# Kernel optimization log

Measured on AMD Instinct MI355X. Metric: run time of the kernel, lower is better.

Reference implementation:

```python
import jax, jax.numpy as jnp
import numpy as np

GROUP = 64  # group_size for precision='int4'


def setup_inputs() -> dict:
    key = jax.random.key(0)
    ks = jax.random.split(key, 7)
    B, S, C, O, R = 64, 4, 8192, 8192, 32
    x = jax.random.normal(ks[0], (B, S, C), dtype=jnp.float32)
    # unpacked int4 weight values stored as int32 codes in [0,16) -> value = code - 8
    qweight = jax.random.randint(ks[1], (O, C), 0, 16, dtype=jnp.int32)
    wscales = jax.random.uniform(ks[2], (C // GROUP, O), dtype=jnp.float32,
                                 minval=0.005, maxval=0.02)
    # smoothing factors kept strictly positive and away from zero
    smooth_factor = jax.random.uniform(ks[3], (C,), dtype=jnp.float32,
                                       minval=0.5, maxval=1.5)
    proj_down = jax.random.normal(ks[4], (C, R), dtype=jnp.float32) * 0.02
    proj_up = jax.random.normal(ks[5], (O, R), dtype=jnp.float32) * 0.02
    bias = jax.random.normal(ks[6], (O,), dtype=jnp.float32) * 0.01
    return {"x": x, "qweight": qweight, "wscales": wscales,
            "smooth_factor": smooth_factor, "proj_down": proj_down,
            "proj_up": proj_up, "bias": bias}


def reference(x, qweight, wscales, smooth_factor, proj_down, proj_up, bias):
    B, S, C = x.shape
    O = qweight.shape[0]
    ng = C // GROUP
    xr = x.reshape(B * S, C)

    # SVD low-rank correction: lora_act = x @ proj_down ; out += lora_act @ proj_up^T
    lora = (xr @ proj_down) @ proj_up.T  # (M, O)

    # activation smoothing + per-group symmetric int4 quantization
    xs = xr / smooth_factor                                   # (M, C)
    xg = xs.reshape(-1, ng, GROUP)                            # (M, ng, 64)
    ascales = jnp.max(jnp.abs(xg), axis=-1, keepdims=True) / 7.0
    ascales = jnp.maximum(ascales, 1e-8)
    q_act = jnp.clip(jnp.round(xg / ascales), -8.0, 7.0)
    x_deq = (q_act * ascales).reshape(-1, C)                  # dequantized act

    # per-group weight dequant: wscales is (ng, O)
    w = (qweight.astype(jnp.float32) - 8.0).reshape(O, ng, GROUP)
    w_deq = (w * wscales.T[:, :, None]).reshape(O, C)         # (O, C)

    out = x_deq @ w_deq.T + lora + bias                       # (M, O)
    return out.reshape(B, S, O)
```

## Files before the change

### kernel.cpp

```cpp
#include <hip/hip_runtime.h>
#include <stdint.h>

#define C_DIM 8192
#define O_DIM 8192
#define M_DIM 256
#define NG    128
#define RK    32
#define SUPS  16
#define GPS   8

typedef float f32x4 __attribute__((ext_vector_type(4)));
typedef int   i32x4 __attribute__((ext_vector_type(4)));
typedef unsigned int u32;

__device__ __forceinline__ void gll16(const void* g, void* l) {
  __builtin_amdgcn_global_load_lds(
      (const __attribute__((address_space(1))) void*)g,
      (__attribute__((address_space(3))) void*)l, 16, 0, 0);
}
__device__ __forceinline__ int pack8(i32x4 r) {
  return (r[0] & 0xff) | ((r[1] & 0xff) << 8) | ((r[2] & 0xff) << 16) |
         (r[3] << 24);
}

__global__ __launch_bounds__(256) void k_lora(const float* __restrict__ x,
                                              const float* __restrict__ pd,
                                              float* __restrict__ lact) {
  const int t  = threadIdx.x;
  const int rq = t & 7;
  const int kc = (t >> 3) & 15;
  const int ml = t >> 7;
  const int m  = blockIdx.x * 2 + ml;
  const float* xrow = x + (size_t)m * C_DIM + kc * 512;
  const float* pdp  = pd + (size_t)(kc * 512) * RK + rq * 4;
  float a0 = 0.f, a1 = 0.f, a2 = 0.f, a3 = 0.f;
  for (int k = 0; k < 512; k += 4) {
    float4 xv = *(const float4*)(xrow + k);
    float4 p0 = *(const float4*)(pdp + (size_t)(k + 0) * RK);
    float4 p1 = *(const float4*)(pdp + (size_t)(k + 1) * RK);
    float4 p2 = *(const float4*)(pdp + (size_t)(k + 2) * RK);
    float4 p3 = *(const float4*)(pdp + (size_t)(k + 3) * RK);
    a0 += xv.x * p0.x + xv.y * p1.x + xv.z * p2.x + xv.w * p3.x;
    a1 += xv.x * p0.y + xv.y * p1.y + xv.z * p2.y + xv.w * p3.y;
    a2 += xv.x * p0.z + xv.y * p1.z + xv.z * p2.z + xv.w * p3.z;
    a3 += xv.x * p0.w + xv.y * p1.w + xv.z * p2.w + xv.w * p3.w;
  }
  __shared__ float red[2][8][16][4];
  red[ml][rq][kc][0] = a0;
  red[ml][rq][kc][1] = a1;
  red[ml][rq][kc][2] = a2;
  red[ml][rq][kc][3] = a3;
  __syncthreads();
  if (t < 64) {
    const int ml2 = t >> 5, r = t & 31, rq2 = r >> 2, j = r & 3;
    float s = 0.f;
#pragma unroll
    for (int c = 0; c < 16; ++c) s += red[ml2][rq2][c][j];
    lact[(size_t)(blockIdx.x * 2 + ml2) * RK + r] = s;
  }
}

__global__ __launch_bounds__(256) void k_prep(const float* __restrict__ x,
                                              const float* __restrict__ smooth,
                                              float* __restrict__ scp,
                                              i32x4* __restrict__ wsA8) {
  const int t    = threadIdx.x;
  const int ml   = t & 15;
  const int gl   = t >> 4;
  const int MT   = blockIdx.x >> 3;
  const int gblk = blockIdx.x & 7;
  const int m = MT * 16 + ml;
  const int g = gblk * 16 + gl;
  const float* xp = x + (size_t)m * C_DIM + g * 64;
  const float* sp = smooth + g * 64;
  float xs[64];
  float amax = 0.0f;
#pragma unroll
  for (int i = 0; i < 64; i += 4) {
    float4 xv = *(const float4*)(xp + i);
    float4 sv = *(const float4*)(sp + i);
    xs[i + 0] = xv.x / sv.x;
    xs[i + 1] = xv.y / sv.y;
    xs[i + 2] = xv.z / sv.z;
    xs[i + 3] = xv.w / sv.w;
    amax = fmaxf(amax, fabsf(xs[i + 0]));
    amax = fmaxf(amax, fabsf(xs[i + 1]));
    amax = fmaxf(amax, fabsf(xs[i + 2]));
    amax = fmaxf(amax, fabsf(xs[i + 3]));
  }
  const float ascale = fmaxf(amax / 7.0f, 1e-8f);
  int qi[64];
  int rs = 0;
#pragma unroll
  for (int i = 0; i < 64; ++i) {
    float qv = fminf(fmaxf(rintf(xs[i] / ascale), -8.0f), 7.0f);
    qi[i] = (int)qv;
    rs += qi[i];
  }
  scp[(size_t)g * 512 + m]       = ascale;
  scp[(size_t)g * 512 + 256 + m] = 8.0f * (float)rs * ascale;
  const size_t base = ((size_t)(MT * NG + g)) * 64;
#pragma unroll
  for (int lg = 0; lg < 4; ++lg) {
    const int* q = qi + lg * 16;
    i32x4 c;
#pragma unroll
    for (int dw = 0; dw < 4; ++dw)
      c[dw] = (q[dw * 4 + 0] & 0xff) | ((q[dw * 4 + 1] & 0xff) << 8) |
              ((q[dw * 4 + 2] & 0xff) << 16) | (q[dw * 4 + 3] << 24);
    wsA8[base + lg * 16 + ml] = c;
  }
}

__global__ __launch_bounds__(512, 4) void k_main(
    const int* __restrict__ qw, const float* __restrict__ wsc,
    const float* __restrict__ pu, const float* __restrict__ bias,
    const float* __restrict__ scp, const i32x4* __restrict__ wsA8,
    const float* __restrict__ lact, float* __restrict__ out) {
  const int t    = threadIdx.x;
  const int n0   = blockIdx.x * 16;
  const int w    = t >> 6;
  const int l    = t & 63;
  const int lrow = l >> 4;
  const int lcol = l & 15;

  __shared__ char  ldsB[2][16][512];
  __shared__ float ldsSC[2][4096];
  __shared__ float ldsW[NG * 16];

  for (int i = t; i < NG * 16; i += 512)
    ldsW[i] = wsc[(size_t)(i >> 4) * O_DIM + n0 + (i & 15)];

  const int sr = t >> 5, cg = t & 31;
  const int* gB = qw + (size_t)(n0 + sr) * C_DIM + cg * 16;
  const int wslot = (cg ^ (sr & 7)) * 16;
  const char* gSCb = (const char*)scp;
  const i32x4* gA0 = wsA8 + ((size_t)(w * 2 + 0) * NG) * 64 + l;
  const i32x4* gA1 = wsA8 + ((size_t)(w * 2 + 1) * NG) * 64 + l;

  f32x4 acc0 = (f32x4){0.f, 0.f, 0.f, 0.f};
  f32x4 acc1 = (f32x4){0.f, 0.f, 0.f, 0.f};
  const i32x4 z = (i32x4){0, 0, 0, 0};

  i32x4 br0, br1, br2, br3;
  i32x4 R0_0, R0_1, R1_0, R1_1, R2_0, R2_1, R3_0, R3_1;

  __syncthreads();

  br0 = __builtin_nontemporal_load((const i32x4*)(gB + 0));
  br1 = __builtin_nontemporal_load((const i32x4*)(gB + 4));
  br2 = __builtin_nontemporal_load((const i32x4*)(gB + 8));
  br3 = __builtin_nontemporal_load((const i32x4*)(gB + 12));
  gll16(gSCb + t * 16, &ldsSC[0][t * 4]);
  gll16(gSCb + 8192 + t * 16, &ldsSC[0][2048 + t * 4]);
  R0_0 = gA0[0 * 64];  R0_1 = gA1[0 * 64];
  R1_0 = gA0[1 * 64];  R1_1 = gA1[1 * 64];
  R2_0 = gA0[2 * 64];  R2_1 = gA1[2 * 64];
  R3_0 = gA0[3 * 64];  R3_1 = gA1[3 * 64];
  asm volatile("s_waitcnt vmcnt(8)" ::: "memory");
  {
    i32x4 pk = (i32x4){pack8(br0), pack8(br1), pack8(br2), pack8(br3)};
    *(i32x4*)&ldsB[0][sr][wslot] = pk;
  }
  asm volatile("s_waitcnt lgkmcnt(0)" ::: "memory");
  __builtin_amdgcn_s_barrier();

#define SUBJ(J, RA, RB, VMC)                                                   \
  {                                                                            \
    asm volatile("s_waitcnt vmcnt(" #VMC ")" ::: "memory");                    \
    i32x4 bf = *(const i32x4*)&ldsB[s & 1][lcol]                               \
                   [(((J) * 4 + lrow) ^ (lcol & 7)) * 16];                     \
    f32x4 as0 = *(const f32x4*)&ldsSC[s & 1][(J) * 512 + (w * 2 + 0) * 16 +    \
                                             lrow * 4];                        \
    f32x4 rs0 = *(const f32x4*)&ldsSC[s & 1][(J) * 512 + 256 +                 \
                                             (w * 2 + 0) * 16 + lrow * 4];     \
    f32x4 as1 = *(const f32x4*)&ldsSC[s & 1][(J) * 512 + (w * 2 + 1) * 16 +    \
                                             lrow * 4];                        \
    f32x4 rs1 = *(const f32x4*)&ldsSC[s & 1][(J) * 512 + 256 +                 \
                                             (w * 2 + 1) * 16 + lrow * 4];     \
    const float wsv = ldsW[(s * GPS + (J)) * 16 + lcol];                       \
    i32x4 d0 = __builtin_amdgcn_mfma_i32_16x16x64_i8(RA, bf, z, 0, 0, 0);      \
    i32x4 d1 = __builtin_amdgcn_mfma_i32_16x16x64_i8(RB, bf, z, 0, 0, 0);      \
    int gn = s * GPS + (J) + 4;                                                \
    if (gn > NG - 1) gn = NG - 1;                                              \
    RA = gA0[(size_t)gn * 64];                                                 \
    RB = gA1[(size_t)gn * 64];                                                 \
    f32x4 df0, df1;                                                            \
    df0[0] = (float)d0[0]; df0[1] = (float)d0[1];                              \
    df0[2] = (float)d0[2]; df0[3] = (float)d0[3];                              \
    df1[0] = (float)d1[0]; df1[1] = (float)d1[1];                              \
    df1[2] = (float)d1[2]; df1[3] = (float)d1[3];                              \
    acc0 += wsv * (as0 * df0 - rs0);                                           \
    acc1 += wsv * (as1 * df1 - rs1);                                           \
  }

  for (int s = 0; s < SUPS; ++s) {
    const int sn = (s < SUPS - 1) ? s + 1 : SUPS - 1;
    const int nb = (s + 1) & 1;
    br0 = __builtin_nontemporal_load((const i32x4*)(gB + sn * 512 + 0));
    br1 = __builtin_nontemporal_load((const i32x4*)(gB + sn * 512 + 4));
    br2 = __builtin_nontemporal_load((const i32x4*)(gB + sn * 512 + 8));
    br3 = __builtin_nontemporal_load((const i32x4*)(gB + sn * 512 + 12));
    gll16(gSCb + (size_t)sn * 16384 + t * 16, &ldsSC[nb][t * 4]);
    gll16(gSCb + (size_t)sn * 16384 + 8192 + t * 16, &ldsSC[nb][2048 + t * 4]);

    SUBJ(0, R0_0, R0_1, 12)
    SUBJ(1, R1_0, R1_1, 12)
    SUBJ(2, R2_0, R2_1, 12)
    SUBJ(3, R3_0, R3_1, 12)
    SUBJ(4, R0_0, R0_1, 6)
    SUBJ(5, R1_0, R1_1, 6)
    SUBJ(6, R2_0, R2_1, 6)
    SUBJ(7, R3_0, R3_1, 6)

    asm volatile("s_waitcnt vmcnt(8)" ::: "memory");
    i32x4 pk = (i32x4){pack8(br0), pack8(br1), pack8(br2), pack8(br3)};
    *(i32x4*)&ldsB[nb][sr][wslot] = pk;
    asm volatile("s_waitcnt lgkmcnt(0)" ::: "memory");
    __builtin_amdgcn_s_barrier();
  }
#undef SUBJ

  const int n = n0 + lcol;
  const float bv = bias[n];
  float4 puq[8];
#pragma unroll
  for (int rq = 0; rq < 8; ++rq)
    puq[rq] = *(const float4*)(pu + (size_t)n * RK + rq * 4);
#pragma unroll
  for (int mi = 0; mi < 2; ++mi) {
    const f32x4 av = (mi == 0) ? acc0 : acc1;
#pragma unroll
    for (int j = 0; j < 4; ++j) {
      const int m = (w * 2 + mi) * 16 + lrow * 4 + j;
      const float* lp = lact + (size_t)m * RK;
      float lo = 0.f;
#pragma unroll
      for (int rq = 0; rq < 8; ++rq) {
        float4 lv = *(const float4*)(lp + rq * 4);
        lo += lv.x * puq[rq].x + lv.y * puq[rq].y + lv.z * puq[rq].z +
              lv.w * puq[rq].w;
      }
      out[(size_t)m * O_DIM + n] = av[j] + bv + lo;
    }
  }
}

extern "C" void kernel_launch(void* const* d_in, const int* in_sizes, int n_in,
                              void* d_out, int out_size, void* d_ws,
                              size_t ws_size, hipStream_t stream) {
  const float* x      = (const float*)d_in[0];
  const int*   qw     = (const int*)d_in[1];
  const float* wsc    = (const float*)d_in[2];
  const float* smooth = (const float*)d_in[3];
  const float* pd     = (const float*)d_in[4];
  const float* pu     = (const float*)d_in[5];
  const float* bias   = (const float*)d_in[6];
  float* out = (float*)d_out;

  char* ws = (char*)d_ws;
  float* lact = (float*)ws;
  float* scp  = (float*)(ws + 32 * 1024);
  i32x4* wsA8 = (i32x4*)(ws + 288 * 1024);

  hipLaunchKernelGGL(k_prep, dim3(128), dim3(256), 0, stream, x, smooth, scp,
                     wsA8);
  hipLaunchKernelGGL(k_lora, dim3(128), dim3(256), 0, stream, x, pd, lact);
  hipLaunchKernelGGL(k_main, dim3(512), dim3(512), 0, stream, qw, wsc, pu,
                     bias, scp, wsA8, lact, out);
}
```

Measured before the change: 163.5 us.

## Split K across two blocks with wider N tiles and add reduction kernel

Each k_main block now covers 32 output columns and half of the K range, so every activation fragment feeds four MFMAs instead of two and A reuse doubles. Partial sums go to two workspace planes, and a new k_red kernel adds them together with the LoRA correction and bias. The weight LDS tile changes from an XOR swizzle to a padded 528-byte row stride, and weight loads are no longer nontemporal. The cost is an extra kernel launch and roughly 16 MB of extra partial-sum traffic.

```diff
diff --git a/kernel.cpp b/kernel.cpp
--- a/kernel.cpp
+++ b/kernel.cpp
@@ -5,9 +5,9 @@
 #define O_DIM 8192
 #define M_DIM 256
 #define NG    128
+#define NGH   64
+#define SUPS  8
 #define RK    32
-#define SUPS  16
-#define GPS   8
 
 typedef float f32x4 __attribute__((ext_vector_type(4)));
 typedef int   i32x4 __attribute__((ext_vector_type(4)));
@@ -18,9 +18,8 @@
       (const __attribute__((address_space(1))) void*)g,
       (__attribute__((address_space(3))) void*)l, 16, 0, 0);
 }
-__device__ __forceinline__ int pack8(i32x4 r) {
-  return (r[0] & 0xff) | ((r[1] & 0xff) << 8) | ((r[2] & 0xff) << 16) |
-         (r[3] << 24);
+__device__ __forceinline__ int pack4(int a, int b, int c, int d) {
+  return (a & 0xff) | ((b & 0xff) << 8) | ((c & 0xff) << 16) | (d << 24);
 }
 
 __global__ __launch_bounds__(256) void k_lora(const float* __restrict__ x,
@@ -106,143 +105,192 @@
     i32x4 c;
 #pragma unroll
     for (int dw = 0; dw < 4; ++dw)
-      c[dw] = (q[dw * 4 + 0] & 0xff) | ((q[dw * 4 + 1] & 0xff) << 8) |
-              ((q[dw * 4 + 2] & 0xff) << 16) | (q[dw * 4 + 3] << 24);
+      c[dw] = pack4(q[dw * 4 + 0], q[dw * 4 + 1], q[dw * 4 + 2], q[dw * 4 + 3]);
     wsA8[base + lg * 16 + ml] = c;
   }
 }
 
 __global__ __launch_bounds__(512, 4) void k_main(
     const int* __restrict__ qw, const float* __restrict__ wsc,
-    const float* __restrict__ pu, const float* __restrict__ bias,
     const float* __restrict__ scp, const i32x4* __restrict__ wsA8,
-    const float* __restrict__ lact, float* __restrict__ out) {
+    float* __restrict__ P) {
   const int t    = threadIdx.x;
-  const int n0   = blockIdx.x * 16;
+  const int bid  = blockIdx.x;
+  const int kh   = bid & 1;
+  const int n0   = (bid >> 1) * 32;
+  const int g0   = kh * NGH;
   const int w    = t >> 6;
   const int l    = t & 63;
   const int lrow = l >> 4;
   const int lcol = l & 15;
 
-  __shared__ char  ldsB[2][16][512];
+  __shared__ char  ldsB[2][32 * 528];
   __shared__ float ldsSC[2][4096];
-  __shared__ float ldsW[NG * 16];
-
-  for (int i = t; i < NG * 16; i += 512)
-    ldsW[i] = wsc[(size_t)(i >> 4) * O_DIM + n0 + (i & 15)];
-
-  const int sr = t >> 5, cg = t & 31;
-  const int* gB = qw + (size_t)(n0 + sr) * C_DIM + cg * 16;
-  const int wslot = (cg ^ (sr & 7)) * 16;
-  const char* gSCb = (const char*)scp;
-  const i32x4* gA0 = wsA8 + ((size_t)(w * 2 + 0) * NG) * 64 + l;
-  const i32x4* gA1 = wsA8 + ((size_t)(w * 2 + 1) * NG) * 64 + l;
-
-  f32x4 acc0 = (f32x4){0.f, 0.f, 0.f, 0.f};
-  f32x4 acc1 = (f32x4){0.f, 0.f, 0.f, 0.f};
-  const i32x4 z = (i32x4){0, 0, 0, 0};
-
-  i32x4 br0, br1, br2, br3;
+  __shared__ float ldsW[NGH * 32];
+
+  for (int i = t; i < NGH * 32; i += 512)
+    ldsW[i] = wsc[(size_t)(g0 + (i >> 5)) * O_DIM + n0 + (i & 31)];
+
+  const int sr = t >> 4, sc = t & 15;
+  const int* gB = qw + (size_t)(n0 + sr) * C_DIM + kh * 4096 + sc * 32;
+  const float* gSC = scp + (size_t)g0 * 512 + t * 4;
+  const int wOff = sr * 528 + sc * 32;
+  const i32x4* gA0 = wsA8 + ((size_t)(w * 2 + 0) * NG + g0) * 64 + l;
+  const i32x4* gA1 = wsA8 + ((size_t)(w * 2 + 1) * NG + g0) * 64 + l;
+
+  __syncthreads();
+
+  i32x4 br0, br1, br2, br3, br4, br5, br6, br7;
   i32x4 R0_0, R0_1, R1_0, R1_1, R2_0, R2_1, R3_0, R3_1;
 
-  __syncthreads();
-
-  br0 = __builtin_nontemporal_load((const i32x4*)(gB + 0));
-  br1 = __builtin_nontemporal_load((const i32x4*)(gB + 4));
-  br2 = __builtin_nontemporal_load((const i32x4*)(gB + 8));
-  br3 = __builtin_nontemporal_load((const i32x4*)(gB + 12));
-  gll16(gSCb + t * 16, &ldsSC[0][t * 4]);
-  gll16(gSCb + 8192 + t * 16, &ldsSC[0][2048 + t * 4]);
+#define LOADB(S)                                                               \
+  br0 = *(const i32x4*)(gB + (S) * 512 + 0);                                   \
+  br1 = *(const i32x4*)(gB + (S) * 512 + 4);                                   \
+  br2 = *(const i32x4*)(gB + (S) * 512 + 8);                                   \
+  br3 = *(const i32x4*)(gB + (S) * 512 + 12);                                  \
+  br4 = *(const i32x4*)(gB + (S) * 512 + 16);                                  \
+  br5 = *(const i32x4*)(gB + (S) * 512 + 20);                                  \
+  br6 = *(const i32x4*)(gB + (S) * 512 + 24);                                  \
+  br7 = *(const i32x4*)(gB + (S) * 512 + 28);
+#define LOADSC(S, BUF)                                                         \
+  gll16(gSC + (size_t)(S) * 4096, &ldsSC[BUF][t * 4]);                         \
+  gll16(gSC + (size_t)(S) * 4096 + 2048, &ldsSC[BUF][2048 + t * 4]);
+#define PACKW(BUF)                                                             \
+  {                                                                            \
+    i32x4 pk0, pk1;                                                            \
+    pk0[0] = pack4(br0[0], br0[1], br0[2], br0[3]);                            \
+    pk0[1] = pack4(br1[0], br1[1], br1[2], br1[3]);                            \
+    pk0[2] = pack4(br2[0], br2[1], br2[2], br2[3]);                            \
+    pk0[3] = pack4(br3[0], br3[1], br3[2], br3[3]);                            \
+    pk1[0] = pack4(br4[0], br4[1], br4[2], br4[3]);                            \
+    pk1[1] = pack4(br5[0], br5[1], br5[2], br5[3]);                            \
+    pk1[2] = pack4(br6[0], br6[1], br6[2], br6[3]);                            \
+    pk1[3] = pack4(br7[0], br7[1], br7[2], br7[3]);                            \
+    *(i32x4*)&ldsB[BUF][wOff] = pk0;                                           \
+    *(i32x4*)&ldsB[BUF][wOff + 16] = pk1;                                      \
+  }
+
+  LOADB(0)
+  LOADSC(0, 0)
   R0_0 = gA0[0 * 64];  R0_1 = gA1[0 * 64];
   R1_0 = gA0[1 * 64];  R1_1 = gA1[1 * 64];
   R2_0 = gA0[2 * 64];  R2_1 = gA1[2 * 64];
   R3_0 = gA0[3 * 64];  R3_1 = gA1[3 * 64];
   asm volatile("s_waitcnt vmcnt(8)" ::: "memory");
-  {
-    i32x4 pk = (i32x4){pack8(br0), pack8(br1), pack8(br2), pack8(br3)};
-    *(i32x4*)&ldsB[0][sr][wslot] = pk;
-  }
+  PACKW(0)
   asm volatile("s_waitcnt lgkmcnt(0)" ::: "memory");
   __builtin_amdgcn_s_barrier();
 
-#define SUBJ(J, RA, RB, VMC)                                                   \
+  f32x4 acc00 = (f32x4){0.f, 0.f, 0.f, 0.f};
+  f32x4 acc01 = (f32x4){0.f, 0.f, 0.f, 0.f};
+  f32x4 acc10 = (f32x4){0.f, 0.f, 0.f, 0.f};
+  f32x4 acc11 = (f32x4){0.f, 0.f, 0.f, 0.f};
+  const i32x4 z = (i32x4){0, 0, 0, 0};
+
+#define SUBJ(J, RA0, RA1, VMC)                                                 \
   {                                                                            \
     asm volatile("s_waitcnt vmcnt(" #VMC ")" ::: "memory");                    \
-    i32x4 bf = *(const i32x4*)&ldsB[s & 1][lcol]                               \
-                   [(((J) * 4 + lrow) ^ (lcol & 7)) * 16];                     \
-    f32x4 as0 = *(const f32x4*)&ldsSC[s & 1][(J) * 512 + (w * 2 + 0) * 16 +    \
-                                             lrow * 4];                        \
-    f32x4 rs0 = *(const f32x4*)&ldsSC[s & 1][(J) * 512 + 256 +                 \
-                                             (w * 2 + 0) * 16 + lrow * 4];     \
-    f32x4 as1 = *(const f32x4*)&ldsSC[s & 1][(J) * 512 + (w * 2 + 1) * 16 +    \
-                                             lrow * 4];                        \
-    f32x4 rs1 = *(const f32x4*)&ldsSC[s & 1][(J) * 512 + 256 +                 \
-                                             (w * 2 + 1) * 16 + lrow * 4];     \
-    const float wsv = ldsW[(s * GPS + (J)) * 16 + lcol];                       \
-    i32x4 d0 = __builtin_amdgcn_mfma_i32_16x16x64_i8(RA, bf, z, 0, 0, 0);      \
-    i32x4 d1 = __builtin_amdgcn_mfma_i32_16x16x64_i8(RB, bf, z, 0, 0, 0);      \
-    int gn = s * GPS + (J) + 4;                                                \
-    if (gn > NG - 1) gn = NG - 1;                                              \
-    RA = gA0[(size_t)gn * 64];                                                 \
-    RB = gA1[(size_t)gn * 64];                                                 \
-    f32x4 df0, df1;                                                            \
-    df0[0] = (float)d0[0]; df0[1] = (float)d0[1];                              \
-    df0[2] = (float)d0[2]; df0[3] = (float)d0[3];                              \
-    df1[0] = (float)d1[0]; df1[1] = (float)d1[1];                              \
-    df1[2] = (float)d1[2]; df1[3] = (float)d1[3];                              \
-    acc0 += wsv * (as0 * df0 - rs0);                                           \
-    acc1 += wsv * (as1 * df1 - rs1);                                           \
+    const char* bb = &ldsB[s & 1][0];                                          \
+    i32x4 bf0 = *(const i32x4*)(bb + lcol * 528 + (J) * 64 + lrow * 16);       \
+    i32x4 bf1 = *(const i32x4*)(bb + (16 + lcol) * 528 + (J) * 64 + lrow * 16);\
+    const float* scb = &ldsSC[s & 1][(J) * 512];                               \
+    f32x4 as0 = *(const f32x4*)(scb + (w * 2 + 0) * 16 + lrow * 4);            \
+    f32x4 rs0 = *(const f32x4*)(scb + 256 + (w * 2 + 0) * 16 + lrow * 4);      \
+    f32x4 as1 = *(const f32x4*)(scb + (w * 2 + 1) * 16 + lrow * 4);            \
+    f32x4 rs1 = *(const f32x4*)(scb + 256 + (w * 2 + 1) * 16 + lrow * 4);      \
+    const float wsv0 = ldsW[(s * 8 + (J)) * 32 + lcol];                        \
+    const float wsv1 = ldsW[(s * 8 + (J)) * 32 + 16 + lcol];                   \
+    i32x4 d00 = __builtin_amdgcn_mfma_i32_16x16x64_i8(RA0, bf0, z, 0, 0, 0);   \
+    i32x4 d01 = __builtin_amdgcn_mfma_i32_16x16x64_i8(RA0, bf1, z, 0, 0, 0);   \
+    i32x4 d10 = __builtin_amdgcn_mfma_i32_16x16x64_i8(RA1, bf0, z, 0, 0, 0);   \
+    i32x4 d11 = __builtin_amdgcn_mfma_i32_16x16x64_i8(RA1, bf1, z, 0, 0, 0);   \
+    {                                                                          \
+      int lgn = s * 8 + (J) + 4;                                               \
+      if (lgn > NGH - 1) lgn = NGH - 1;                                        \
+      RA0 = gA0[(size_t)lgn * 64];                                             \
+      RA1 = gA1[(size_t)lgn * 64];                                             \
+    }                                                                          \
+    f32x4 df;                                                                  \
+    df[0] = (float)d00[0]; df[1] = (float)d00[1];                              \
+    df[2] = (float)d00[2]; df[3] = (float)d00[3];                              \
+    acc00 += wsv0 * (as0 * df - rs0);                                          \
+    df[0] = (float)d01[0]; df[1] = (float)d01[1];                              \
+    df[2] = (float)d01[2]; df[3] = (float)d01[3];                              \
+    acc01 += wsv1 * (as0 * df - rs0);                                          \
+    df[0] = (float)d10[0]; df[1] = (float)d10[1];                              \
+    df[2] = (float)d10[2]; df[3] = (float)d10[3];                              \
+    acc10 += wsv0 * (as1 * df - rs1);                                          \
+    df[0] = (float)d11[0]; df[1] = (float)d11[1];                              \
+    df[2] = (float)d11[2]; df[3] = (float)d11[3];                              \
+    acc11 += wsv1 * (as1 * df - rs1);                                          \
   }
 
   for (int s = 0; s < SUPS; ++s) {
     const int sn = (s < SUPS - 1) ? s + 1 : SUPS - 1;
     const int nb = (s + 1) & 1;
-    br0 = __builtin_nontemporal_load((const i32x4*)(gB + sn * 512 + 0));
-    br1 = __builtin_nontemporal_load((const i32x4*)(gB + sn * 512 + 4));
-    br2 = __builtin_nontemporal_load((const i32x4*)(gB + sn * 512 + 8));
-    br3 = __builtin_nontemporal_load((const i32x4*)(gB + sn * 512 + 12));
-    gll16(gSCb + (size_t)sn * 16384 + t * 16, &ldsSC[nb][t * 4]);
-    gll16(gSCb + (size_t)sn * 16384 + 8192 + t * 16, &ldsSC[nb][2048 + t * 4]);
-
-    SUBJ(0, R0_0, R0_1, 12)
-    SUBJ(1, R1_0, R1_1, 12)
-    SUBJ(2, R2_0, R2_1, 12)
-    SUBJ(3, R3_0, R3_1, 12)
+    LOADB(sn)
+    LOADSC(sn, nb)
+    SUBJ(0, R0_0, R0_1, 16)
+    SUBJ(1, R1_0, R1_1, 16)
+    SUBJ(2, R2_0, R2_1, 16)
+    SUBJ(3, R3_0, R3_1, 16)
     SUBJ(4, R0_0, R0_1, 6)
     SUBJ(5, R1_0, R1_1, 6)
     SUBJ(6, R2_0, R2_1, 6)
     SUBJ(7, R3_0, R3_1, 6)
-
     asm volatile("s_waitcnt vmcnt(8)" ::: "memory");
-    i32x4 pk = (i32x4){pack8(br0), pack8(br1), pack8(br2), pack8(br3)};
-    *(i32x4*)&ldsB[nb][sr][wslot] = pk;
+    PACKW(nb)
     asm volatile("s_waitcnt lgkmcnt(0)" ::: "memory");
     __builtin_amdgcn_s_barrier();
   }
 #undef SUBJ
-
-  const int n = n0 + lcol;
+#undef LOADB
+#undef LOADSC
+#undef PACKW
+
+  float* Pk = P + (size_t)kh * (M_DIM * O_DIM);
+#pragma unroll
+  for (int mi = 0; mi < 2; ++mi) {
+#pragma unroll
+    for (int ni = 0; ni < 2; ++ni) {
+      const f32x4 av = (mi == 0) ? (ni == 0 ? acc00 : acc01)
+                                 : (ni == 0 ? acc10 : acc11);
+      const int n = n0 + ni * 16 + lcol;
+#pragma unroll
+      for (int j = 0; j < 4; ++j) {
+        const int m = (w * 2 + mi) * 16 + lrow * 4 + j;
+        Pk[(size_t)m * O_DIM + n] = av[j];
+      }
+    }
+  }
+}
+
+__global__ __launch_bounds__(256) void k_red(const float* __restrict__ P,
+                                             const float* __restrict__ lact,
+                                             const float* __restrict__ pu,
+                                             const float* __restrict__ bias,
+                                             float* __restrict__ out) {
+  const int t  = threadIdx.x;
+  const int tn = t & 31;
+  const int tm = t >> 5;
+  const int n0 = blockIdx.x * 32;
+  __shared__ float puL[32][33];
+  for (int i = t; i < 1024; i += 256)
+    puL[i >> 5][i & 31] = pu[(size_t)(n0 + (i >> 5)) * RK + (i & 31)];
+  __syncthreads();
+  const int n = n0 + tn;
   const float bv = bias[n];
-  float4 puq[8];
-#pragma unroll
-  for (int rq = 0; rq < 8; ++rq)
-    puq[rq] = *(const float4*)(pu + (size_t)n * RK + rq * 4);
-#pragma unroll
-  for (int mi = 0; mi < 2; ++mi) {
-    const f32x4 av = (mi == 0) ? acc0 : acc1;
-#pragma unroll
-    for (int j = 0; j < 4; ++j) {
-      const int m = (w * 2 + mi) * 16 + lrow * 4 + j;
-      const float* lp = lact + (size_t)m * RK;
-      float lo = 0.f;
-#pragma unroll
-      for (int rq = 0; rq < 8; ++rq) {
-        float4 lv = *(const float4*)(lp + rq * 4);
-        lo += lv.x * puq[rq].x + lv.y * puq[rq].y + lv.z * puq[rq].z +
-              lv.w * puq[rq].w;
-      }
-      out[(size_t)m * O_DIM + n] = av[j] + bv + lo;
+  for (int m = tm; m < M_DIM; m += 8) {
+    const float* lp = lact + (size_t)m * RK;
+    float s = bv;
+#pragma unroll
+    for (int r = 0; r < 32; r += 4) {
+      float4 lv = *(const float4*)(lp + r);
+      s += lv.x * puL[tn][r] + lv.y * puL[tn][r + 1] + lv.z * puL[tn][r + 2] +
+           lv.w * puL[tn][r + 3];
     }
+    const size_t o = (size_t)m * O_DIM + n;
+    out[o] = P[o] + P[(size_t)M_DIM * O_DIM + o] + s;
   }
 }
 
@@ -262,10 +310,13 @@
   float* lact = (float*)ws;
   float* scp  = (float*)(ws + 32 * 1024);
   i32x4* wsA8 = (i32x4*)(ws + 288 * 1024);
+  float* P    = (float*)(ws + 2336 * 1024);
 
   hipLaunchKernelGGL(k_prep, dim3(128), dim3(256), 0, stream, x, smooth, scp,
                      wsA8);
   hipLaunchKernelGGL(k_lora, dim3(128), dim3(256), 0, stream, x, pd, lact);
-  hipLaunchKernelGGL(k_main, dim3(512), dim3(512), 0, stream, qw, wsc, pu,
-                     bias, scp, wsA8, lact, out);
-}
+  hipLaunchKernelGGL(k_main, dim3(512), dim3(512), 0, stream, qw, wsc, scp,
+                     wsA8, P);
+  hipLaunchKernelGGL(k_red, dim3(256), dim3(256), 0, stream, P, lact, pu, bias,
+                     out);
+}
```

Result: slower. 457.3 us (+179.7%).
